# Kernel optimization log

Hardware: AMD Instinct MI355X
Metric: run time of the kernel (lower is better)

Reference implementation:

```python
import jax, jax.numpy as jnp
import numpy as np

B, T, C, H = 128, 256, 384, 6
HS = C // H  # 64
EPS = 1e-5


def _ln(x, g, b):
    mu = jnp.mean(x, axis=-1, keepdims=True)
    var = jnp.mean(jnp.square(x - mu), axis=-1, keepdims=True)
    return (x - mu) * jax.lax.rsqrt(var + EPS) * g + b


def setup_inputs() -> dict:
    key = jax.random.key(0)
    ks = jax.random.split(key, 12)
    s = 0.02
    return {
        "x": jax.random.normal(ks[0], (B, T, C), jnp.float32),
        "wq": jax.random.normal(ks[1], (H, C, HS), jnp.float32) * s,
        "wk": jax.random.normal(ks[2], (H, C, HS), jnp.float32) * s,
        "wv": jax.random.normal(ks[3], (H, C, HS), jnp.float32) * s,
        "w_proj": jax.random.normal(ks[4], (C, C), jnp.float32) * s,
        "b_proj": jax.random.normal(ks[5], (C,), jnp.float32) * s,
        "w1": jax.random.normal(ks[6], (C, 4 * C), jnp.float32) * s,
        "b1": jax.random.normal(ks[7], (4 * C,), jnp.float32) * s,
        "w2": jax.random.normal(ks[8], (4 * C, C), jnp.float32) * s,
        "b2": jax.random.normal(ks[9], (C,), jnp.float32) * s,
        "ln1_g": 1.0 + jax.random.normal(ks[10], (C,), jnp.float32) * s,
        "ln1_b": jnp.zeros((C,), jnp.float32),
        "ln2_g": 1.0 + jax.random.normal(ks[11], (C,), jnp.float32) * s,
        "ln2_b": jnp.zeros((C,), jnp.float32),
    }


def reference(x, wq, wk, wv, w_proj, b_proj, w1, b1, w2, b2, ln1_g, ln1_b, ln2_g, ln2_b):
    # --- attention sublayer (dropout = identity, eval mode) ---
    h = _ln(x, ln1_g, ln1_b)                              # (B,T,C)
    q = jnp.einsum("btc,hcd->bhtd", h, wq)               # (B,H,T,HS)
    k = jnp.einsum("btc,hcd->bhtd", h, wk)
    v = jnp.einsum("btc,hcd->bhtd", h, wv)
    # NOTE: original scales by n_embed**-0.5 (C), not head_size**-0.5
    wei = jnp.einsum("bhtd,bhsd->bhts", q, k) * (C ** -0.5)  # (B,H,T,T)
    tril = jnp.tril(jnp.ones((T, T), bool))
    wei = jnp.where(tril, wei, -jnp.inf)
    # NOTE: original applies softmax over torch dim=1 of (B,T,T) = query axis
    wei = jax.nn.softmax(wei, axis=2)
    attn = jnp.einsum("bhts,bhsd->bhtd", wei, v)          # (B,H,T,HS)
    attn = attn.transpose(0, 2, 1, 3).reshape(B, T, C)    # head-concat order
    x = x + attn @ w_proj + b_proj
    # --- MLP sublayer ---
    h2 = _ln(x, ln2_g, ln2_b)
    x = x + jax.nn.relu(h2 @ w1 + b1) @ w2 + b2
    return x
```

## Files before the change

kernel.cpp:

```cpp
#include <hip/hip_runtime.h>

#define BB 128
#define TT 256
#define CCH 384
#define NHH 6
#define HSZ 64
#define BTT (BB*TT)
#define QKVLD 1152

typedef unsigned short u16;
typedef unsigned int   u32;
typedef __attribute__((ext_vector_type(8))) short  short8;
typedef __attribute__((ext_vector_type(4))) float  floatx4;

__device__ __forceinline__ u16 f2bf(float f) {
  union { float f; u32 i; } v; v.f = f; u32 x = v.i;
  return (u16)((x + 0x7fffu + ((x >> 16) & 1u)) >> 16);
}
__device__ __forceinline__ float bf2f(u16 w) {
  union { u32 i; float f; } v; v.i = ((u32)w) << 16; return v.f;
}

__device__ __forceinline__ void gll16(const u16* g, u16* l) {
  __builtin_amdgcn_global_load_lds((const __attribute__((address_space(1))) void*)g,
                                   (__attribute__((address_space(3))) void*)l, 16, 0, 0);
}

template <int INBF>
__global__ __launch_bounds__(256) void ln_kernel(const void* __restrict__ xv,
                                                 const float* __restrict__ g,
                                                 const float* __restrict__ b,
                                                 u16* __restrict__ out) {
  int row = blockIdx.x * 4 + (threadIdx.x >> 6);
  int lane = threadIdx.x & 63;
  float vals[6];
  float sum = 0.f;
  if (INBF) {
    const u16* xr = (const u16*)xv + (size_t)row * CCH;
#pragma unroll
    for (int i = 0; i < 6; ++i) { vals[i] = bf2f(xr[lane + (i << 6)]); sum += vals[i]; }
  } else {
    const float* xr = (const float*)xv + (size_t)row * CCH;
#pragma unroll
    for (int i = 0; i < 6; ++i) { vals[i] = xr[lane + (i << 6)]; sum += vals[i]; }
  }
#pragma unroll
  for (int off = 32; off; off >>= 1) sum += __shfl_xor(sum, off);
  float mean = sum * (1.f / 384.f);
  float vs = 0.f;
#pragma unroll
  for (int i = 0; i < 6; ++i) { float d = vals[i] - mean; vs += d * d; }
#pragma unroll
  for (int off = 32; off; off >>= 1) vs += __shfl_xor(vs, off);
  float rinv = rsqrtf(vs * (1.f / 384.f) + 1e-5f);
  u16* orow = out + (size_t)row * CCH;
#pragma unroll
  for (int i = 0; i < 6; ++i) {
    int c = lane + (i << 6);
    orow[c] = f2bf((vals[i] - mean) * rinv * g[c] + b[c]);
  }
}

__global__ void repack_all(const float* __restrict__ wq, const float* __restrict__ wk,
                           const float* __restrict__ wv, const float* __restrict__ wproj,
                           const float* __restrict__ w1, const float* __restrict__ w2,
                           u16* __restrict__ wqkv_t, u16* __restrict__ wp_t,
                           u16* __restrict__ w1_t, u16* __restrict__ w2_t) {
  int idx = blockIdx.x * 256 + threadIdx.x;
  const int S1 = 442368;
  const int S2 = S1 + 147456;
  const int S3 = S2 + 589824;
  const int S4 = S3 + 589824;
  if (idx < S1) {
    int i = idx, e = i & 7, l = (i >> 3) & 63, r = i >> 9;
    int kt = r % 12, nb = r / 12;
    int n = nb * 16 + (l & 15), k = kt * 32 + (l >> 4) * 8 + e;
    int sel = n / 384, nn = n % 384;
    size_t src = ((size_t)(nn >> 6) * 384 + k) * 64 + (nn & 63);
    float v = (sel == 0) ? wq[src] : (sel == 1) ? wk[src] : wv[src];
    wqkv_t[i] = f2bf(v);
  } else if (idx < S2) {
    int i = idx - S1, e = i & 7, l = (i >> 3) & 63, r = i >> 9;
    int kt = r % 12, nb = r / 12;
    int n = nb * 16 + (l & 15), k = kt * 32 + (l >> 4) * 8 + e;
    wp_t[i] = f2bf(wproj[(size_t)k * 384 + n]);
  } else if (idx < S3) {
    int i = idx - S2, e = i & 7, l = (i >> 3) & 63, r = i >> 9;
    int kt = r % 12, nb = r / 12;
    int n = nb * 16 + (l & 15), k = kt * 32 + (l >> 4) * 8 + e;
    w1_t[i] = f2bf(w1[(size_t)k * 1536 + n]);
  } else if (idx < S4) {
    int i = idx - S3, e = i & 7, l = (i >> 3) & 63, r = i >> 9;
    int kt = r % 48, nb = r / 48;
    int n = nb * 16 + (l & 15), k = kt * 32 + (l >> 4) * 8 + e;
    w2_t[i] = f2bf(w2[(size_t)k * 384 + n]);
  }
}

template <int BIAS, int RES, int RELU, int OUTBF, int RESBF>
__global__ __launch_bounds__(192, 2) void gemm_kres3(const u16* __restrict__ A,
                                                     const u16* __restrict__ Bp,
                                                     const float* __restrict__ bias,
                                                     const void* __restrict__ resv,
                                                     void* __restrict__ outv,
                                                     int M, int N) {
  __shared__ __align__(16) u16 Ah[12 * 2048];
  const int tid = threadIdx.x;
  const int lane = tid & 63;
  const int w = tid >> 6;

  const int gx = gridDim.x;
  const int nwg = gx * gridDim.y;
  const int bid = blockIdx.y * gx + blockIdx.x;
  const int lin = (bid & 7) * (nwg >> 3) + (bid >> 3);
  const int m0 = (lin / gx) * 64, n0 = (lin % gx) * 192;

  const int lm = lane & 15, qd = lane >> 4;

#pragma unroll
  for (int g = 0; g < 16; ++g) {
    int call = w * 16 + g;
    int kt = call >> 2, c = call & 3;
    int row = 16 * c + (lane >> 2);
    int ch = (lane & 3) ^ ((row >> 1) & 3);
    const u16* src = A + (size_t)(m0 + row) * 384 + kt * 32 + ch * 8;
    gll16(src, &Ah[kt * 2048 + c * 512]);
  }

  const u16* bsrc[4];
#pragma unroll
  for (int j = 0; j < 4; ++j)
    bsrc[j] = Bp + ((size_t)((n0 >> 4) + 4 * w + j) * 12) * 512 + lane * 8;

  floatx4 acc[4][4];
  floatx4 zero4 = {0.f, 0.f, 0.f, 0.f};
#pragma unroll
  for (int i = 0; i < 4; ++i)
#pragma unroll
    for (int j = 0; j < 4; ++j) acc[i][j] = zero4;

  short8 bf[3][4];
#pragma unroll
  for (int j = 0; j < 4; ++j) bf[0][j] = *(const short8*)(bsrc[j]);
#pragma unroll
  for (int j = 0; j < 4; ++j) bf[1][j] = *(const short8*)(bsrc[j] + 512);

  asm volatile("s_waitcnt vmcnt(0)" ::: "memory");
  __syncthreads();

#pragma unroll
  for (int kt = 0; kt < 12; ++kt) {
    if (kt + 2 < 12) {
      const int pb = (kt + 2) % 3;
#pragma unroll
      for (int j = 0; j < 4; ++j)
        bf[pb][j] = *(const short8*)(bsrc[j] + (kt + 2) * 512);
    }
    const int cb = kt % 3;
    short8 af[4];
#pragma unroll
    for (int i = 0; i < 4; ++i) {
      int rm = 16 * i + lm;
      af[i] = *(const short8*)&Ah[kt * 2048 + rm * 32 + (qd ^ ((rm >> 1) & 3)) * 8];
    }
#pragma unroll
    for (int i = 0; i < 4; ++i)
#pragma unroll
      for (int j = 0; j < 4; ++j)
        acc[i][j] = __builtin_amdgcn_mfma_f32_16x16x32_bf16(af[i], bf[cb][j], acc[i][j], 0, 0, 0);
  }

#pragma unroll
  for (int i = 0; i < 4; ++i) {
    int row0 = m0 + 16 * i + qd * 4;
#pragma unroll
    for (int j = 0; j < 4; ++j) {
      int col = n0 + 64 * w + 16 * j + lm;
      float bb = 0.f;
      if (BIAS) bb = bias[col];
#pragma unroll
      for (int r = 0; r < 4; ++r) {
        size_t idx = (size_t)(row0 + r) * N + col;
        float val = acc[i][j][r] + bb;
        if (RES) val += RESBF ? bf2f(((const u16*)resv)[idx]) : ((const float*)resv)[idx];
        if (RELU) val = fmaxf(val, 0.f);
        if (OUTBF) ((u16*)outv)[idx] = f2bf(val);
        else       ((float*)outv)[idx] = val;
      }
    }
  }
}

template <int BIAS, int RES, int RELU, int OUTBF, int RESBF>
__global__ __launch_bounds__(256, 3) void gemm_mfma(const u16* __restrict__ A,
                                                    const u16* __restrict__ Bp,
                                                    const float* __restrict__ bias,
                                                    const void* __restrict__ resv,
                                                    void* __restrict__ outv,
                                                    int M, int N, int K) {
  __shared__ __align__(16) u16 As[2][128 * 32];
  const int tid = threadIdx.x;
  const int lane = tid & 63;
  const int w = tid >> 6;
  const int wr = w >> 1, wc = w & 1;

  const int gx = gridDim.x;
  const int nwg = gx * gridDim.y;
  const int bid = blockIdx.y * gx + blockIdx.x;
  const int lin = (bid & 7) * (nwg >> 3) + (bid >> 3);
  const int m0 = (lin / gx) * 128, n0 = (lin % gx) * 128;

  const int lm = lane & 15, qd = lane >> 4;
  const int KT = K >> 5;

  floatx4 acc[4][4];
  floatx4 zero4 = {0.f, 0.f, 0.f, 0.f};
#pragma unroll
  for (int i = 0; i < 4; ++i)
#pragma unroll
    for (int j = 0; j < 4; ++j) acc[i][j] = zero4;

  const u16* srcA[2];
#pragma unroll
  for (int c = 0; c < 2; ++c) {
    int row = 32 * w + 16 * c + (lane >> 2);
    int ch = (lane & 3) ^ ((row >> 1) & 3);
    srcA[c] = A + (size_t)(m0 + row) * K + ch * 8;
  }
  const int dA = (32 * w) * 32;

  const u16* bsrc[4];
#pragma unroll
  for (int j = 0; j < 4; ++j)
    bsrc[j] = Bp + ((size_t)((n0 >> 4) + 4 * wc + j) * KT) * 512 + lane * 8;

#pragma unroll
  for (int c = 0; c < 2; ++c) gll16(srcA[c], &As[0][dA + 512 * c]);
  short8 bcur[4], bnxt[4];
#pragma unroll
  for (int j = 0; j < 4; ++j) bcur[j] = *(const short8*)(bsrc[j]);

  for (int k0 = 0; k0 < K; k0 += 64) {
    __syncthreads();
    {
      int kn = k0 + 32;
      int kto = (kn >> 5) << 9;
#pragma unroll
      for (int j = 0; j < 4; ++j) bnxt[j] = *(const short8*)(bsrc[j] + kto);
#pragma unroll
      for (int c = 0; c < 2; ++c) gll16(srcA[c] + kn, &As[1][dA + 512 * c]);
      short8 af[4];
#pragma unroll
      for (int i = 0; i < 4; ++i) {
        int rm = 64 * wr + 16 * i + lm;
        af[i] = *(const short8*)&As[0][rm * 32 + (qd ^ ((rm >> 1) & 3)) * 8];
      }
#pragma unroll
      for (int i = 0; i < 4; ++i)
#pragma unroll
        for (int j = 0; j < 4; ++j)
          acc[i][j] = __builtin_amdgcn_mfma_f32_16x16x32_bf16(af[i], bcur[j], acc[i][j], 0, 0, 0);
    }
    __syncthreads();
    {
      int kn = k0 + 64;
      if (kn < K) {
        int kto = (kn >> 5) << 9;
#pragma unroll
        for (int j = 0; j < 4; ++j) bcur[j] = *(const short8*)(bsrc[j] + kto);
#pragma unroll
        for (int c = 0; c < 2; ++c) gll16(srcA[c] + kn, &As[0][dA + 512 * c]);
      }
      short8 af[4];
#pragma unroll
      for (int i = 0; i < 4; ++i) {
        int rm = 64 * wr + 16 * i + lm;
        af[i] = *(const short8*)&As[1][rm * 32 + (qd ^ ((rm >> 1) & 3)) * 8];
      }
#pragma unroll
      for (int i = 0; i < 4; ++i)
#pragma unroll
        for (int j = 0; j < 4; ++j)
          acc[i][j] = __builtin_amdgcn_mfma_f32_16x16x32_bf16(af[i], bnxt[j], acc[i][j], 0, 0, 0);
    }
  }

#pragma unroll
  for (int i = 0; i < 4; ++i) {
    int row0 = m0 + 64 * wr + 16 * i + qd * 4;
#pragma unroll
    for (int j = 0; j < 4; ++j) {
      int col = n0 + 64 * wc + 16 * j + lm;
      float bb = 0.f;
      if (BIAS) bb = bias[col];
#pragma unroll
      for (int r = 0; r < 4; ++r) {
        size_t idx = (size_t)(row0 + r) * N + col;
        float val = acc[i][j][r] + bb;
        if (RES) val += RESBF ? bf2f(((const u16*)resv)[idx]) : ((const float*)resv)[idx];
        if (RELU) val = fmaxf(val, 0.f);
        if (OUTBF) ((u16*)outv)[idx] = f2bf(val);
        else       ((float*)outv)[idx] = val;
      }
    }
  }
}

#define ASCALE 0.051031036307982884f

__global__ __launch_bounds__(1024) void attn_mfma(const u16* __restrict__ qkv,
                                                  u16* __restrict__ out) {
  __shared__ __align__(16) char lds_raw[36864 + 20480 + 2048];
  u16*   Ks       = (u16*)lds_raw;
  u16*   VT       = (u16*)lds_raw;
  float* partials = (float*)(lds_raw + 36864);
  u16*   stage    = (u16*)(lds_raw + 36864);
  float* gmax     = (float*)(lds_raw + 57344);
  float* linv     = (float*)(lds_raw + 58368);

  const int tid = threadIdx.x;
  const int lane = tid & 63;
  const int w = tid >> 6;
  const int lm = lane & 15, qd = lane >> 4;
  const int b = blockIdx.x / NHH, h = blockIdx.x % NHH;
  const size_t rowbase = (size_t)b * TT;
  const u16* qp = qkv + rowbase * QKVLD + h * HSZ;
  const u16* kp = qp + 384;
  const u16* vp = qp + 768;

  {
    int s = tid >> 2, c4 = tid & 3;
    const u16* src = kp + (size_t)s * QKVLD;
    *(uint4*)&Ks[s * 72 + c4 * 8]       = *(const uint4*)(src + c4 * 8);
    *(uint4*)&Ks[s * 72 + (c4 + 4) * 8] = *(const uint4*)(src + (c4 + 4) * 8);
  }
  short8 qf0, qf1;
  {
    const u16* qrow = qp + (size_t)(16 * w + lm) * QKVLD + qd * 8;
    qf0 = *(const short8*)(qrow);
    qf1 = *(const short8*)(qrow + 32);
  }
  __syncthreads();

  floatx4 acc[16];
  floatx4 zero4 = {0.f, 0.f, 0.f, 0.f};
#pragma unroll
  for (int tc = 0; tc < 16; ++tc) acc[tc] = zero4;

#pragma unroll
  for (int tc = 0; tc < 16; ++tc) {
    if (tc <= w) {
      int sr = 16 * tc + lm;
      short8 kf0 = *(const short8*)&Ks[sr * 72 + qd * 8];
      short8 kf1 = *(const short8*)&Ks[sr * 72 + 32 + qd * 8];
      acc[tc] = __builtin_amdgcn_mfma_f32_16x16x32_bf16(qf0, kf0, acc[tc], 0, 0, 0);
      acc[tc] = __builtin_amdgcn_mfma_f32_16x16x32_bf16(qf1, kf1, acc[tc], 0, 0, 0);
    }
  }

  const int rb = 16 * w + qd * 4;
  float pmax[16];
#pragma unroll
  for (int tc = 0; tc < 16; ++tc) {
    float m = -1e30f;
    if (tc <= w) {
      int sc = 16 * tc + lm;
#pragma unroll
      for (int r = 0; r < 4; ++r) {
        float vv = acc[tc][r] * ASCALE;
        vv = (rb + r >= sc) ? vv : -1e30f;
        acc[tc][r] = vv;
        m = fmaxf(m, vv);
      }
    }
    m = fmaxf(m, __shfl_xor(m, 16));
    m = fmaxf(m, __shfl_xor(m, 32));
    pmax[tc] = m;
  }
  if (lane < 16) {
#pragma unroll
    for (int tc = 0; tc < 16; ++tc) partials[w * 256 + tc * 16 + lane] = pmax[tc];
  }
  __syncthreads();
  if (tid < 256) {
    float m = partials[tid];
#pragma unroll
    for (int i = 1; i < 16; ++i) m = fmaxf(m, partials[i * 256 + tid]);
    gmax[tid] = m;
  }
  __syncthreads();

  float psum[16];
#pragma unroll
  for (int tc = 0; tc < 16; ++tc) {
    float s = 0.f;
    if (tc <= w) {
      float gm = gmax[tc * 16 + lm];
#pragma unroll
      for (int r = 0; r < 4; ++r) {
        float e = (acc[tc][r] > -1e29f) ? __expf(acc[tc][r] - gm) : 0.f;
        acc[tc][r] = e;
        s += e;
      }
    }
    s += __shfl_xor(s, 16);
    s += __shfl_xor(s, 32);
    psum[tc] = s;
  }
  if (lane < 16) {
#pragma unroll
    for (int tc = 0; tc < 16; ++tc) partials[w * 256 + tc * 16 + lane] = psum[tc];
  }
  __syncthreads();
  if (tid < 256) {
    float s = partials[tid];
#pragma unroll
    for (int i = 1; i < 16; ++i) s += partials[i * 256 + tid];
    linv[tid] = 1.f / s;
  }
  __syncthreads();

  {
    int s = tid >> 2, dg = (tid & 3) * 16;
    const u16* vrow = vp + (size_t)s * QKVLD + dg;
    u16 tmp[16];
    *(uint4*)&tmp[0] = *(const uint4*)(vrow);
    *(uint4*)&tmp[8] = *(const uint4*)(vrow + 8);
#pragma unroll
    for (int j = 0; j < 16; ++j) VT[(dg + j) * 264 + s] = tmp[j];
  }
  __syncthreads();

  u16* mst = stage + w * 640;
  floatx4 oacc[4];
#pragma unroll
  for (int nt = 0; nt < 4; ++nt) oacc[nt] = zero4;

#pragma unroll
  for (int c = 0; c < 8; ++c) {
    if (2 * c <= w) {
#pragma unroll
      for (int tt = 0; tt < 2; ++tt) {
        int tc = 2 * c + tt;
        float li = (tc <= w) ? linv[tc * 16 + lm] : 0.f;
#pragma unroll
        for (int r = 0; r < 4; ++r) {
          float pv = (tc <= w) ? acc[tc][r] * li : 0.f;
          mst[(qd * 4 + r) * 40 + tt * 16 + lm] = f2bf(pv);
        }
      }
      asm volatile("s_waitcnt lgkmcnt(0)" ::: "memory");
      short8 pf = *(const short8*)&mst[lm * 40 + qd * 8];
#pragma unroll
      for (int nt = 0; nt < 4; ++nt) {
        short8 vf = *(const short8*)&VT[(nt * 16 + lm) * 264 + c * 32 + qd * 8];
        oacc[nt] = __builtin_amdgcn_mfma_f32_16x16x32_bf16(pf, vf, oacc[nt], 0, 0, 0);
      }
      asm volatile("" ::: "memory");
    }
  }

  u16* ob = out + rowbase * CCH + h * HSZ;
#pragma unroll
  for (int nt = 0; nt < 4; ++nt) {
#pragma unroll
    for (int r = 0; r < 4; ++r) {
      int t = 16 * w + qd * 4 + r;
      ob[(size_t)t * CCH + nt * 16 + lm] = f2bf(oacc[nt][r]);
    }
  }
}

extern "C" void kernel_launch(void* const* d_in, const int* in_sizes, int n_in,
                              void* d_out, int out_size, void* d_ws, size_t ws_size,
                              hipStream_t stream) {
  const float* x     = (const float*)d_in[0];
  const float* wq    = (const float*)d_in[1];
  const float* wk    = (const float*)d_in[2];
  const float* wv    = (const float*)d_in[3];
  const float* wproj = (const float*)d_in[4];
  const float* bproj = (const float*)d_in[5];
  const float* w1    = (const float*)d_in[6];
  const float* b1    = (const float*)d_in[7];
  const float* w2    = (const float*)d_in[8];
  const float* b2    = (const float*)d_in[9];
  const float* ln1g  = (const float*)d_in[10];
  const float* ln1b  = (const float*)d_in[11];
  const float* ln2g  = (const float*)d_in[12];
  const float* ln2b  = (const float*)d_in[13];
  float* out = (float*)d_out;
  (void)in_sizes; (void)n_in; (void)out_size; (void)ws_size;

  char* ws = (char*)d_ws;
  size_t off = 0;
  auto alloc = [&](size_t bytes) -> void* {
    void* p = ws + off;
    off += (bytes + 255) & ~(size_t)255;
    return p;
  };

  u16* wqkv_t = (u16*)alloc((size_t)QKVLD * CCH * 2);
  u16* wp_t   = (u16*)alloc((size_t)CCH * CCH * 2);
  u16* w1_t   = (u16*)alloc((size_t)4 * CCH * CCH * 2);
  u16* w2_t   = (u16*)alloc((size_t)CCH * 4 * CCH * 2);
  u16*   h_b  = (u16*)alloc((size_t)BTT * CCH * 2);
  u16*   x2   = (u16*)alloc((size_t)BTT * CCH * 2);
  u16*   qkv_b = (u16*)alloc((size_t)BTT * 4 * CCH * 2);
  u16*   u_b   = qkv_b;

  repack_all<<<6912, 256, 0, stream>>>(wq, wk, wv, wproj, w1, w2,
                                       wqkv_t, wp_t, w1_t, w2_t);

  ln_kernel<0><<<BTT / 4, 256, 0, stream>>>(x, ln1g, ln1b, h_b);

  gemm_kres3<0, 0, 0, 1, 0><<<dim3(6, 512), 192, 0, stream>>>(h_b, wqkv_t, nullptr, nullptr,
                                                              qkv_b, BTT, QKVLD);
  attn_mfma<<<BB * NHH, 1024, 0, stream>>>(qkv_b, h_b);

  gemm_kres3<1, 1, 0, 1, 0><<<dim3(2, 512), 192, 0, stream>>>(h_b, wp_t, bproj, x, x2,
                                                              BTT, CCH);
  ln_kernel<1><<<BTT / 4, 256, 0, stream>>>(x2, ln2g, ln2b, h_b);

  gemm_kres3<1, 0, 1, 1, 0><<<dim3(8, 512), 192, 0, stream>>>(h_b, w1_t, b1, nullptr, u_b,
                                                              BTT, 4 * CCH);
  gemm_mfma<1, 1, 0, 0, 1><<<dim3(3, 256), 256, 0, stream>>>(u_b, w2_t, b2, x2, out,
                                                             BTT, CCH, 4 * CCH);
}
```

Baseline: 338.6 us.

## Fuse weight repack with first LayerNorm and deepen B prefetch in gemm

The weight repack kernel and the first LayerNorm kernel are merged into one launch, with extra blocks past the repack range doing the LN rows. This removes one launch and lets the two independent jobs overlap on the device. The gemm_kres3 B-fragment register ring is also widened from 3 to 4 stages so loads are issued three k-tiles ahead. That adds register pressure under the 2-waves-per-SIMD launch bound.

```diff
diff --git a/kernel.cpp b/kernel.cpp
--- a/kernel.cpp
+++ b/kernel.cpp
@@ -61,39 +61,72 @@
   }
 }
 
-__global__ void repack_all(const float* __restrict__ wq, const float* __restrict__ wk,
-                           const float* __restrict__ wv, const float* __restrict__ wproj,
-                           const float* __restrict__ w1, const float* __restrict__ w2,
-                           u16* __restrict__ wqkv_t, u16* __restrict__ wp_t,
-                           u16* __restrict__ w1_t, u16* __restrict__ w2_t) {
-  int idx = blockIdx.x * 256 + threadIdx.x;
-  const int S1 = 442368;
-  const int S2 = S1 + 147456;
-  const int S3 = S2 + 589824;
-  const int S4 = S3 + 589824;
-  if (idx < S1) {
-    int i = idx, e = i & 7, l = (i >> 3) & 63, r = i >> 9;
-    int kt = r % 12, nb = r / 12;
-    int n = nb * 16 + (l & 15), k = kt * 32 + (l >> 4) * 8 + e;
-    int sel = n / 384, nn = n % 384;
-    size_t src = ((size_t)(nn >> 6) * 384 + k) * 64 + (nn & 63);
-    float v = (sel == 0) ? wq[src] : (sel == 1) ? wk[src] : wv[src];
-    wqkv_t[i] = f2bf(v);
-  } else if (idx < S2) {
-    int i = idx - S1, e = i & 7, l = (i >> 3) & 63, r = i >> 9;
-    int kt = r % 12, nb = r / 12;
-    int n = nb * 16 + (l & 15), k = kt * 32 + (l >> 4) * 8 + e;
-    wp_t[i] = f2bf(wproj[(size_t)k * 384 + n]);
-  } else if (idx < S3) {
-    int i = idx - S2, e = i & 7, l = (i >> 3) & 63, r = i >> 9;
-    int kt = r % 12, nb = r / 12;
-    int n = nb * 16 + (l & 15), k = kt * 32 + (l >> 4) * 8 + e;
-    w1_t[i] = f2bf(w1[(size_t)k * 1536 + n]);
-  } else if (idx < S4) {
-    int i = idx - S3, e = i & 7, l = (i >> 3) & 63, r = i >> 9;
-    int kt = r % 48, nb = r / 48;
-    int n = nb * 16 + (l & 15), k = kt * 32 + (l >> 4) * 8 + e;
-    w2_t[i] = f2bf(w2[(size_t)k * 384 + n]);
+__global__ __launch_bounds__(256) void prep_all(const float* __restrict__ wq,
+                                                const float* __restrict__ wk,
+                                                const float* __restrict__ wv,
+                                                const float* __restrict__ wproj,
+                                                const float* __restrict__ w1,
+                                                const float* __restrict__ w2,
+                                                u16* __restrict__ wqkv_t, u16* __restrict__ wp_t,
+                                                u16* __restrict__ w1_t, u16* __restrict__ w2_t,
+                                                const float* __restrict__ x,
+                                                const float* __restrict__ ln1g,
+                                                const float* __restrict__ ln1b,
+                                                u16* __restrict__ h_out) {
+  const int bidx = blockIdx.x;
+  if (bidx < 6912) {
+    int idx = bidx * 256 + threadIdx.x;
+    const int S1 = 442368;
+    const int S2 = S1 + 147456;
+    const int S3 = S2 + 589824;
+    const int S4 = S3 + 589824;
+    if (idx < S1) {
+      int i = idx, e = i & 7, l = (i >> 3) & 63, r = i >> 9;
+      int kt = r % 12, nb = r / 12;
+      int n = nb * 16 + (l & 15), k = kt * 32 + (l >> 4) * 8 + e;
+      int sel = n / 384, nn = n % 384;
+      size_t src = ((size_t)(nn >> 6) * 384 + k) * 64 + (nn & 63);
+      float v = (sel == 0) ? wq[src] : (sel == 1) ? wk[src] : wv[src];
+      wqkv_t[i] = f2bf(v);
+    } else if (idx < S2) {
+      int i = idx - S1, e = i & 7, l = (i >> 3) & 63, r = i >> 9;
+      int kt = r % 12, nb = r / 12;
+      int n = nb * 16 + (l & 15), k = kt * 32 + (l >> 4) * 8 + e;
+      wp_t[i] = f2bf(wproj[(size_t)k * 384 + n]);
+    } else if (idx < S3) {
+      int i = idx - S2, e = i & 7, l = (i >> 3) & 63, r = i >> 9;
+      int kt = r % 12, nb = r / 12;
+      int n = nb * 16 + (l & 15), k = kt * 32 + (l >> 4) * 8 + e;
+      w1_t[i] = f2bf(w1[(size_t)k * 1536 + n]);
+    } else if (idx < S4) {
+      int i = idx - S3, e = i & 7, l = (i >> 3) & 63, r = i >> 9;
+      int kt = r % 48, nb = r / 48;
+      int n = nb * 16 + (l & 15), k = kt * 32 + (l >> 4) * 8 + e;
+      w2_t[i] = f2bf(w2[(size_t)k * 384 + n]);
+    }
+  } else {
+    int row = (bidx - 6912) * 4 + (threadIdx.x >> 6);
+    int lane = threadIdx.x & 63;
+    const float* xr = x + (size_t)row * CCH;
+    float vals[6];
+    float sum = 0.f;
+#pragma unroll
+    for (int i = 0; i < 6; ++i) { vals[i] = xr[lane + (i << 6)]; sum += vals[i]; }
+#pragma unroll
+    for (int off = 32; off; off >>= 1) sum += __shfl_xor(sum, off);
+    float mean = sum * (1.f / 384.f);
+    float vs = 0.f;
+#pragma unroll
+    for (int i = 0; i < 6; ++i) { float d = vals[i] - mean; vs += d * d; }
+#pragma unroll
+    for (int off = 32; off; off >>= 1) vs += __shfl_xor(vs, off);
+    float rinv = rsqrtf(vs * (1.f / 384.f) + 1e-5f);
+    u16* orow = h_out + (size_t)row * CCH;
+#pragma unroll
+    for (int i = 0; i < 6; ++i) {
+      int c = lane + (i << 6);
+      orow[c] = f2bf((vals[i] - mean) * rinv * ln1g[c] + ln1b[c]);
+    }
   }
 }
 
@@ -139,24 +172,26 @@
 #pragma unroll
     for (int j = 0; j < 4; ++j) acc[i][j] = zero4;
 
-  short8 bf[3][4];
+  short8 bf[4][4];
 #pragma unroll
   for (int j = 0; j < 4; ++j) bf[0][j] = *(const short8*)(bsrc[j]);
 #pragma unroll
   for (int j = 0; j < 4; ++j) bf[1][j] = *(const short8*)(bsrc[j] + 512);
+#pragma unroll
+  for (int j = 0; j < 4; ++j) bf[2][j] = *(const short8*)(bsrc[j] + 1024);
 
   asm volatile("s_waitcnt vmcnt(0)" ::: "memory");
   __syncthreads();
 
 #pragma unroll
   for (int kt = 0; kt < 12; ++kt) {
-    if (kt + 2 < 12) {
-      const int pb = (kt + 2) % 3;
+    if (kt + 3 < 12) {
+      const int pb = (kt + 3) & 3;
 #pragma unroll
       for (int j = 0; j < 4; ++j)
-        bf[pb][j] = *(const short8*)(bsrc[j] + (kt + 2) * 512);
-    }
-    const int cb = kt % 3;
+        bf[pb][j] = *(const short8*)(bsrc[j] + (kt + 3) * 512);
+    }
+    const int cb = kt & 3;
     short8 af[4];
 #pragma unroll
     for (int i = 0; i < 4; ++i) {
@@ -508,10 +543,9 @@
   u16*   qkv_b = (u16*)alloc((size_t)BTT * 4 * CCH * 2);
   u16*   u_b   = qkv_b;
 
-  repack_all<<<6912, 256, 0, stream>>>(wq, wk, wv, wproj, w1, w2,
-                                       wqkv_t, wp_t, w1_t, w2_t);
-
-  ln_kernel<0><<<BTT / 4, 256, 0, stream>>>(x, ln1g, ln1b, h_b);
+  prep_all<<<15104, 256, 0, stream>>>(wq, wk, wv, wproj, w1, w2,
+                                      wqkv_t, wp_t, w1_t, w2_t,
+                                      x, ln1g, ln1b, h_b);
 
   gemm_kres3<0, 0, 0, 1, 0><<<dim3(6, 512), 192, 0, stream>>>(h_b, wqkv_t, nullptr, nullptr,
                                                               qkv_b, BTT, QKVLD);
```

Measured after the change: 335.0 us. No clear change (-1.1%).
